# Kernel tuning notes

Hardware: AMD Instinct MI355X
Metric: run time of the kernel (lower is better)

## Reference

```python
import jax, jax.numpy as jnp
import numpy as np

HIDDEN = 512
WINDOW = 32   # window_size: keys span [i-W, i+W]
HEADS = 8
B = 192       # must equal S for the original torch code to run
S = 192


def _split_heads(x, H):
    b, s, e = x.shape
    return x.reshape(b, s, H, e // H)


def _local_window_attn(q, k, v, W):
    """Sliding-window attention: query i attends keys [i-W, i+W] (clipped).
    q,k,v: (B, S, H, D). Chunked (3-neighbor) formulation: K/V duplicated 3x,
    never (2W+1)x. Requires S % W == 0."""
    B_, S_, H_, D_ = q.shape
    C = W
    nc = S_ // C
    qc = q.reshape(B_, nc, C, H_, D_)
    kc = k.reshape(B_, nc, C, H_, D_)
    vc = v.reshape(B_, nc, C, H_, D_)
    pad = ((0, 0), (1, 1), (0, 0), (0, 0), (0, 0))
    kp = jnp.pad(kc, pad)
    vp = jnp.pad(vc, pad)
    # each query chunk sees chunks [n-1, n, n+1] -> (B, nc, 3C, H, D)
    k3 = jnp.concatenate([kp[:, :-2], kp[:, 1:-1], kp[:, 2:]], axis=2)
    v3 = jnp.concatenate([vp[:, :-2], vp[:, 1:-1], vp[:, 2:]], axis=2)
    scale = 1.0 / np.sqrt(D_)
    scores = jnp.einsum('bnqhd,bnkhd->bnhqk', qc, k3) * scale  # (B,nc,H,C,3C)
    # relative key position = (kk - C) - q, independent of chunk index
    rel = jnp.arange(3 * C)[None, :] - C - jnp.arange(C)[:, None]   # (C, 3C)
    band = (rel >= -W) & (rel <= W)
    k_abs = (jnp.arange(nc)[:, None] - 1) * C + jnp.arange(3 * C)[None, :]  # (nc, 3C)
    inb = (k_abs >= 0) & (k_abs < S_)
    valid = band[None, :, :] & inb[:, None, :]                      # (nc, C, 3C)
    scores = jnp.where(valid[:, None, :, :], scores, -jnp.inf)
    attn = jax.nn.softmax(scores, axis=-1)
    out = jnp.einsum('bnhqk,bnkhd->bnqhd', attn, v3)
    return out.reshape(B_, S_, H_ * D_)


def _forward(hidden_states, h_in_w, h_in_b, h_out_w, h_out_b,
             v_in_w, v_in_b, v_out_w, v_out_b,
             mlp_w1, mlp_b1, mlp_w2, mlp_b2):
    x = hidden_states
    W, H = WINDOW, HEADS
    # vertical attention: window slides over the sequence axis (dim 1)
    qv, kv, vv = jnp.split(x @ v_in_w.T + v_in_b, 3, axis=-1)
    v_ctx = _local_window_attn(_split_heads(qv, H), _split_heads(kv, H),
                               _split_heads(vv, H), W)
    v_out = v_ctx @ v_out_w.T + v_out_b
    # horizontal attention: the original slices hidden_states[start:end]
    # (dim 0), so keys for MHA-batch n are x[i-W:i+W+1, n]. Equivalent to
    # sliding-window attention on the (0,1)-transposed K/V (valid since B==S).
    qh, kh, vh = jnp.split(x @ h_in_w.T + h_in_b, 3, axis=-1)
    h_ctx = _local_window_attn(_split_heads(qh, H),
                               _split_heads(kh.swapaxes(0, 1), H),
                               _split_heads(vh.swapaxes(0, 1), H), W)
    h_out = h_ctx @ h_out_w.T + h_out_b
    combined = jnp.concatenate([h_out, v_out], axis=-1)   # (B, S, 2E)
    hid = jax.nn.relu(combined @ mlp_w1.T + mlp_b1)
    return hid @ mlp_w2.T + mlp_b2                         # (B, S, E)


def setup_inputs() -> dict:
    key = jax.random.key(0)
    ks = jax.random.split(key, 8)
    E = HIDDEN
    def w(k, shape):
        return jax.random.normal(k, shape, dtype=jnp.float32) * 0.02
    return {
        'hidden_states': jax.random.normal(ks[0], (B, S, E), dtype=jnp.float32),
        'h_in_w': w(ks[1], (3 * E, E)), 'h_in_b': jnp.zeros((3 * E,), jnp.float32),
        'h_out_w': w(ks[2], (E, E)), 'h_out_b': jnp.zeros((E,), jnp.float32),
        'v_in_w': w(ks[3], (3 * E, E)), 'v_in_b': jnp.zeros((3 * E,), jnp.float32),
        'v_out_w': w(ks[4], (E, E)), 'v_out_b': jnp.zeros((E,), jnp.float32),
        'mlp_w1': w(ks[5], (E, 2 * E)), 'mlp_b1': jnp.zeros((E,), jnp.float32),
        'mlp_w2': w(ks[6], (E, E)), 'mlp_b2': jnp.zeros((E,), jnp.float32),
    }


def reference(hidden_states, h_in_w, h_in_b, h_out_w, h_out_b,
              v_in_w, v_in_b, v_out_w, v_out_b,
              mlp_w1, mlp_b1, mlp_w2, mlp_b2):
    return _forward(hidden_states, h_in_w, h_in_b, h_out_w, h_out_b,
                    v_in_w, v_in_b, v_out_w, v_out_b,
                    mlp_w1, mlp_b1, mlp_w2, mlp_b2)
```

## Files before the change

### kernel.cpp

```cpp
#include <hip/hip_runtime.h>

typedef __bf16 bf16x8 __attribute__((ext_vector_type(8)));
typedef __bf16 bf16x4 __attribute__((ext_vector_type(4)));
typedef float f32x4 __attribute__((ext_vector_type(4)));

__device__ __forceinline__ float bf2f(unsigned short u) {
  union { unsigned int i; float f; } v; v.i = ((unsigned int)u) << 16; return v.f;
}
__device__ __forceinline__ unsigned short f2bf(float f) {
  union { float f; unsigned int i; } v; v.f = f;
  unsigned int u = v.i;
  u += 0x7fffu + ((u >> 16) & 1u);
  return (unsigned short)(u >> 16);
}

#define SB()  __builtin_amdgcn_sched_barrier(0)
#define BAR() __builtin_amdgcn_s_barrier()

__global__ void cvt_all(const float* __restrict__ x,
                        const float* __restrict__ wv, const float* __restrict__ wh,
                        const float* __restrict__ w1, const float* __restrict__ w2,
                        const float* __restrict__ who, const float* __restrict__ wvo,
                        unsigned short* __restrict__ xb, unsigned short* __restrict__ xt,
                        unsigned short* __restrict__ wvb, unsigned short* __restrict__ whb,
                        unsigned short* __restrict__ w1b, unsigned short* __restrict__ w2b,
                        unsigned short* __restrict__ whoT, unsigned short* __restrict__ wvoT)
{
  const int bid = blockIdx.x;
  const int t = threadIdx.x;
  if (bid < 18432) {
    const int ro = bid * 2 + (t >> 7);
    const int idx = t & 127;
    const int s = ro / 192, b = ro - s * 192;
    const int ri = b * 192 + s;
    float4 v = *(const float4*)&x[(size_t)ri * 512 + idx * 4];
    ushort4 o;
    o.x = f2bf(v.x); o.y = f2bf(v.y); o.z = f2bf(v.z); o.w = f2bf(v.w);
    *(ushort4*)&xb[(size_t)ri * 512 + idx * 4] = o;
    *(ushort4*)&xt[(size_t)ro * 512 + idx * 4] = o;
  } else if (bid < 20736) {
    int q = (bid - 18432) * 256 + t;
    const float* src; unsigned short* dst;
    if (q < 196608)      { src = wv;  dst = wvb; }
    else if (q < 393216) { src = wh;  dst = whb; q -= 196608; }
    else if (q < 524288) { src = w1;  dst = w1b; q -= 393216; }
    else                 { src = w2;  dst = w2b; q -= 524288; }
    float4 v = ((const float4*)src)[q];
    ushort4 o;
    o.x = f2bf(v.x); o.y = f2bf(v.y); o.z = f2bf(v.z); o.w = f2bf(v.w);
    ((ushort4*)dst)[q] = o;
  } else {
    const int tb = bid - 20736;
    const float* src = (tb < 256) ? who : wvo;
    unsigned short* dst = (tb < 256) ? whoT : wvoT;
    const int j = (tb & 255) * 2 + (t >> 7);
    const int i0 = (t & 127) * 4;
    ushort4 o;
    o.x = f2bf(src[(size_t)(i0 + 0) * 512 + j]);
    o.y = f2bf(src[(size_t)(i0 + 1) * 512 + j]);
    o.z = f2bf(src[(size_t)(i0 + 2) * 512 + j]);
    o.w = f2bf(src[(size_t)(i0 + 3) * 512 + j]);
    *(ushort4*)&dst[(size_t)j * 512 + i0] = o;
  }
}

__device__ __forceinline__ void async16(const void* g, void* s) {
  __builtin_amdgcn_global_load_lds(
      (const __attribute__((address_space(1))) unsigned int*)g,
      (__attribute__((address_space(3))) unsigned int*)s, 16, 0, 0);
}

__device__ __forceinline__ void fuse_bias_core(int bid,
    const float* b1, const float* hob, const float* vob,
    const float* w1, float* bf)
{
  const int gid = bid * 256 + (int)threadIdx.x;
  const int o = gid >> 4, g = gid & 15;
  if (o < 512) {
    const float* row = w1 + (size_t)o * 1024;
    float s = 0.f;
    #pragma unroll 8
    for (int m = g * 32; m < g * 32 + 32; ++m) s += row[m] * hob[m];
    #pragma unroll 8
    for (int m = g * 32; m < g * 32 + 32; ++m) s += row[512 + m] * vob[m];
    s += __shfl_xor(s, 1);
    s += __shfl_xor(s, 2);
    s += __shfl_xor(s, 4);
    s += __shfl_xor(s, 8);
    if (g == 0) bf[o] = s + b1[o];
  }
}

template<int OUTF32, int RELU, int MODE, int ADDB>
__device__ __forceinline__ void gemm_core(int bid0, int nwg,
    unsigned short* As, unsigned short* Bs,
    const unsigned short* A, const unsigned short* Bt, void* Cv, const float* bias,
    int M, int N, int K, int lda, int ldb, int ldC, int colOff)
{
  const int per = nwg >> 3;
  const int lb = (bid0 & 7) * per + (bid0 >> 3);
  int tm, tn, batch = 0;
  if (MODE == 1) {
    batch = lb >> 3;
    const int sub = lb & 7;
    tm = sub & 3;
    tn = sub >> 2;
  } else {
    const int nb = N >> 7;
    const int grp = lb / (4 * nb);
    const int r = lb - grp * 4 * nb;
    tm = grp * 4 + (r & 3);
    tn = r >> 2;
  }
  const int t = threadIdx.x;
  const int w = t >> 6, l = t & 63;
  const int wr = w >> 1, wc = w & 1;
  const int lr = l & 15, kg = l >> 4;

  const unsigned short* Abase = A + (size_t)tm * 128 * lda;
  const unsigned short* Bbase = (MODE == 1)
      ? Bt + ((size_t)batch * 192 + tn * 64) * ldb
      : Bt + (size_t)tn * 128 * ldb;

  const int r0 = t >> 2;
  const int s0 = (((t & 3) ^ ((t >> 3) & 3))) * 8;
  const size_t ga0 = (size_t)r0 * lda + s0;
  const size_t ga1 = (size_t)(64 + r0) * lda + s0;
  const size_t gb0 = (size_t)r0 * ldb + s0;
  const size_t gb1 = (size_t)(64 + r0) * ldb + s0;
  const int ldsoff = w * 512;

  const f32x4 zero4 = {0.f, 0.f, 0.f, 0.f};
  f32x4 acc[4][4];
  #pragma unroll
  for (int m = 0; m < 4; ++m)
    #pragma unroll
    for (int n = 0; n < 4; ++n) acc[m][n] = zero4;

  auto stage = [&](int kt, int slot) {
    async16(Abase + ga0 + kt, &As[slot * 4096 + ldsoff]);
    async16(Abase + ga1 + kt, &As[slot * 4096 + 2048 + ldsoff]);
    async16(Bbase + gb0 + kt, &Bs[slot * 4096 + ldsoff]);
    async16(Bbase + gb1 + kt, &Bs[slot * 4096 + 2048 + ldsoff]);
  };

  const int nk = K >> 5;
  stage(0, 0);
  stage(32, 1);

  const int rsw = (kg ^ ((lr >> 1) & 3)) * 8;

  int cur = 0;
  for (int it = 0; it < nk; ++it) {
    if (it + 1 < nk) asm volatile("s_waitcnt vmcnt(4)" ::: "memory");
    else             asm volatile("s_waitcnt vmcnt(0)" ::: "memory");
    SB(); BAR(); SB();

    int st = cur + 2; if (st >= 3) st -= 3;
    if (it + 2 < nk) stage((it + 2) << 5, st);

    bf16x8 af[4], bfv[4];
    #pragma unroll
    for (int m = 0; m < 4; ++m)
      af[m] = *(const bf16x8*)&As[cur * 4096 + (wr * 64 + m * 16 + lr) * 32 + rsw];
    #pragma unroll
    for (int n = 0; n < 4; ++n)
      bfv[n] = *(const bf16x8*)&Bs[cur * 4096 + (wc * 64 + n * 16 + lr) * 32 + rsw];
    #pragma unroll
    for (int m = 0; m < 4; ++m)
      #pragma unroll
      for (int n = 0; n < 4; ++n)
        acc[m][n] = __builtin_amdgcn_mfma_f32_16x16x32_bf16(af[m], bfv[n],
                                                            acc[m][n], 0, 0, 0);
    cur = cur + 1; if (cur >= 3) cur = 0;
  }

  const int row0 = tm * 128 + wr * 64;
  const int colL0 = (MODE == 1) ? (tn * 64 + wc * 64) : (tn * 128 + wc * 64);

  if (MODE == 1) {
    unsigned short* Cw = (unsigned short*)Cv + (size_t)batch * 98304;
    #pragma unroll
    for (int m = 0; m < 4; ++m) {
      const int rowb = row0 + m * 16 + kg * 4;
      float4 bv4 = {0.f, 0.f, 0.f, 0.f};
      if (ADDB) bv4 = *(const float4*)&bias[rowb];
      #pragma unroll
      for (int rr = 0; rr < 4; ++rr) {
        const float bv = ((const float*)&bv4)[rr];
        const size_t rbase = (size_t)(rowb + rr) * 192;
        #pragma unroll
        for (int n = 0; n < 4; ++n) {
          const int j = colL0 + n * 16 + lr;
          Cw[rbase + j] = f2bf(acc[m][n][rr] + bv);
        }
      }
    }
    return;
  }

  #pragma unroll
  for (int n = 0; n < 4; ++n) {
    const int ccol = colL0 + n * 16 + lr;
    const float bv = ADDB ? bias[ccol] : 0.f;
    #pragma unroll
    for (int m = 0; m < 4; ++m) {
      #pragma unroll
      for (int r = 0; r < 4; ++r) {
        const int crow = row0 + m * 16 + kg * 4 + r;
        float v = acc[m][n][r] + bv;
        if (RELU) v = fmaxf(v, 0.f);
        if (OUTF32)
          ((float*)Cv)[(size_t)crow * ldC + colOff + ccol] = v;
        else
          ((unsigned short*)Cv)[(size_t)crow * ldC + colOff + ccol] = f2bf(v);
      }
    }
  }
}

template<int OUTF32, int RELU, int MODE, int ADDB>
__global__ __launch_bounds__(256, 3)
void gemm_bt(const unsigned short* __restrict__ A,
             const unsigned short* __restrict__ Bt,
             void* __restrict__ Cv, const float* __restrict__ bias,
             int M, int N, int K, int lda, int ldb, int ldC, int colOff)
{
  __shared__ unsigned short smem[3 * 4096 * 2];
  gemm_core<OUTF32, RELU, MODE, ADDB>((int)blockIdx.x, (int)gridDim.x,
                                      smem, smem + 12288,
                                      A, Bt, Cv, bias, M, N, K, lda, ldb, ldC, colOff);
}

__global__ __launch_bounds__(256, 3)
void proj_h(const unsigned short* __restrict__ xb, const unsigned short* __restrict__ xt,
            const unsigned short* __restrict__ whb,
            const unsigned short* __restrict__ w1b,
            const unsigned short* __restrict__ whoT, const unsigned short* __restrict__ wvoT,
            unsigned short* __restrict__ vto, unsigned short* __restrict__ qko,
            unsigned short* __restrict__ G, float* __restrict__ bfz,
            const float* __restrict__ h_in_b,
            const float* __restrict__ b1, const float* __restrict__ hob,
            const float* __restrict__ vob, const float* __restrict__ w1f)
{
  __shared__ unsigned short smem[3 * 4096 * 2];
  const int bid = (int)blockIdx.x;
  if (bid < 1536)
    gemm_core<0,0,1,1>(bid, 1536, smem, smem + 12288, whb + 1024 * 512, xt, vto,
                       h_in_b + 1024, 512, 192, 512, 512, 512, 192, 0);
  else if (bid < 3840)
    gemm_core<0,0,0,1>(bid - 1536, 2304, smem, smem + 12288, xb, whb, qko,
                       h_in_b, 36864, 1024, 512, 512, 512, 1024, 0);
  else if (bid < 3856)
    gemm_core<0,0,0,0>(bid - 3840, 16, smem, smem + 12288, w1b, whoT, G,
                       bfz, 512, 512, 512, 1024, 512, 1024, 0);
  else if (bid < 3872)
    gemm_core<0,0,0,0>(bid - 3856, 16, smem, smem + 12288, w1b + 512, wvoT, G,
                       bfz, 512, 512, 512, 1024, 512, 1024, 512);
  else
    fuse_bias_core(bid - 3872, b1, hob, vob, w1f, bfz);
}

__global__ __launch_bounds__(256, 3)
void proj_v(const unsigned short* __restrict__ xb,
            const unsigned short* __restrict__ wvb,
            unsigned short* __restrict__ vto, unsigned short* __restrict__ qko,
            const float* __restrict__ v_in_b)
{
  __shared__ unsigned short smem[3 * 4096 * 2];
  const int bid = (int)blockIdx.x;
  if (bid < 1536)
    gemm_core<0,0,1,1>(bid, 1536, smem, smem + 12288, wvb + 1024 * 512, xb, vto,
                       v_in_b + 1024, 512, 192, 512, 512, 512, 192, 0);
  else
    gemm_core<0,0,0,1>(bid - 1536, 2304, smem, smem + 12288, xb, wvb, qko,
                       v_in_b, 36864, 1024, 512, 512, 512, 1024, 0);
}

__global__ __launch_bounds__(256)
void attn_mfma(const unsigned short* __restrict__ qk,
               const unsigned short* __restrict__ vt,
               unsigned short* __restrict__ ctx, int hbranch, int ldc, int colOff)
{
  __shared__ unsigned short P_lds[4][32 * 104];
  __shared__ float rinv[4][32];

  const int t = threadIdx.x;
  const int w = t >> 6, l = t & 63;
  const int lr = l & 15, kg = l >> 4;
  const int bid = blockIdx.x;
  const int hg = bid & 1;
  const int n = (bid >> 1) % 6;
  const int b = bid / 12;
  const int h = hg * 4 + w;
  const int kabase = (n - 1) * 32;

  bf16x8 qf[2][2];
  #pragma unroll
  for (int ct = 0; ct < 2; ++ct)
    #pragma unroll
    for (int ks = 0; ks < 2; ++ks)
      qf[ct][ks] = *(const bf16x8*)&qk[(size_t)(b * 192 + n * 32 + ct * 16 + lr) * 1024
                                       + h * 64 + ks * 32 + kg * 8];

  const f32x4 z4 = {0.f, 0.f, 0.f, 0.f};
  f32x4 sacc[6][2];
  #pragma unroll
  for (int mt = 0; mt < 6; ++mt) { sacc[mt][0] = z4; sacc[mt][1] = z4; }

  #pragma unroll
  for (int mt = 0; mt < 6; ++mt) {
    int ka = kabase + mt * 16 + lr;
    ka = ka < 0 ? 0 : (ka > 191 ? 191 : ka);
    const size_t row = hbranch ? (size_t)ka * 192 + b : (size_t)b * 192 + ka;
    #pragma unroll
    for (int ks = 0; ks < 2; ++ks) {
      bf16x8 kf = *(const bf16x8*)&qk[row * 1024 + 512 + h * 64 + ks * 32 + kg * 8];
      #pragma unroll
      for (int ct = 0; ct < 2; ++ct)
        sacc[mt][ct] = __builtin_amdgcn_mfma_f32_16x16x32_bf16(kf, qf[ct][ks],
                                                               sacc[mt][ct], 0, 0, 0);
    }
  }

  bf16x8 vf[4][3];
  #pragma unroll
  for (int dt = 0; dt < 4; ++dt)
    #pragma unroll
    for (int t2 = 0; t2 < 3; ++t2) {
      int ka0 = kabase + t2 * 32 + kg * 8;
      if (ka0 < 0 || ka0 > 184) ka0 = 0;
      vf[dt][t2] = *(const bf16x8*)&vt[((size_t)(b * 8 + h) * 64 + dt * 16 + lr) * 192 + ka0];
    }

  unsigned short* Pw = &P_lds[w][0];
  #pragma unroll
  for (int ct = 0; ct < 2; ++ct) {
    const int q = ct * 16 + lr;
    float mx = -1e30f;
    #pragma unroll
    for (int mt = 0; mt < 6; ++mt)
      #pragma unroll
      for (int rr = 0; rr < 4; ++rr) {
        const int kk = mt * 16 + kg * 4 + rr;
        const int ka = kabase + kk;
        const bool valid = (kk >= q) && (kk <= q + 64) && (ka >= 0) && (ka < 192);
        const float s = valid ? sacc[mt][ct][rr] : -1e30f;
        sacc[mt][ct][rr] = s;
        mx = fmaxf(mx, s);
      }
    mx = fmaxf(mx, __shfl_xor(mx, 16));
    mx = fmaxf(mx, __shfl_xor(mx, 32));
    float sum = 0.f;
    #pragma unroll
    for (int mt = 0; mt < 6; ++mt) {
      bf16x4 pk;
      #pragma unroll
      for (int rr = 0; rr < 4; ++rr) {
        const float e = exp2f((sacc[mt][ct][rr] - mx) * 0.1803368801111137f);
        sum += e;
        pk[rr] = (__bf16)e;
      }
      *(bf16x4*)&Pw[q * 104 + mt * 16 + kg * 4] = pk;
    }
    sum += __shfl_xor(sum, 16);
    sum += __shfl_xor(sum, 32);
    if (kg == 0) rinv[w][q] = 1.0f / sum;
  }

  f32x4 oacc[2][4];
  #pragma unroll
  for (int mq = 0; mq < 2; ++mq)
    #pragma unroll
    for (int dt = 0; dt < 4; ++dt) oacc[mq][dt] = z4;

  #pragma unroll
  for (int t2 = 0; t2 < 3; ++t2)
    #pragma unroll
    for (int mq = 0; mq < 2; ++mq) {
      bf16x8 pa = *(const bf16x8*)&Pw[(mq * 16 + lr) * 104 + t2 * 32 + kg * 8];
      #pragma unroll
      for (int dt = 0; dt < 4; ++dt)
        oacc[mq][dt] = __builtin_amdgcn_mfma_f32_16x16x32_bf16(pa, vf[dt][t2],
                                                               oacc[mq][dt], 0, 0, 0);
    }

  #pragma unroll
  for (int mq = 0; mq < 2; ++mq)
    #pragma unroll
    for (int rr = 0; rr < 4; ++rr) {
      const int q = mq * 16 + kg * 4 + rr;
      const float rv = rinv[w][q];
      const size_t row = (size_t)(b * 192 + n * 32 + q) * ldc + colOff + h * 64;
      #pragma unroll
      for (int dt = 0; dt < 4; ++dt)
        ctx[row + dt * 16 + lr] = f2bf(oacc[mq][dt][rr] * rv);
    }
}

extern "C" void kernel_launch(void* const* d_in, const int* in_sizes, int n_in,
                              void* d_out, int out_size, void* d_ws, size_t ws_size,
                              hipStream_t stream) {
  const float* x       = (const float*)d_in[0];
  const float* h_in_w  = (const float*)d_in[1];
  const float* h_in_b  = (const float*)d_in[2];
  const float* h_out_w = (const float*)d_in[3];
  const float* h_out_b = (const float*)d_in[4];
  const float* v_in_w  = (const float*)d_in[5];
  const float* v_in_b  = (const float*)d_in[6];
  const float* v_out_w = (const float*)d_in[7];
  const float* v_out_b = (const float*)d_in[8];
  const float* w1      = (const float*)d_in[9];
  const float* b1      = (const float*)d_in[10];
  const float* w2      = (const float*)d_in[11];
  const float* b2      = (const float*)d_in[12];

  const size_t XB   = 0;
  const size_t WVB  = 37748736;
  const size_t WHB  = 39321600;
  const size_t WHOT = 40894464;
  const size_t WVOT = 41418752;
  const size_t W1B  = 41943040;
  const size_t W2B  = 42991616;
  const size_t CTX2 = 43515904;
  const size_t QKO  = 119013376;
  const size_t VTO  = 194510848;
  const size_t NEED = 232259584;
  if (ws_size < NEED) return;

  char* ws = (char*)d_ws;
  unsigned short* xb   = (unsigned short*)(ws + XB);
  unsigned short* wvb  = (unsigned short*)(ws + WVB);
  unsigned short* whb  = (unsigned short*)(ws + WHB);
  unsigned short* whoT = (unsigned short*)(ws + WHOT);
  unsigned short* wvoT = (unsigned short*)(ws + WVOT);
  unsigned short* w1b  = (unsigned short*)(ws + W1B);
  unsigned short* w2b  = (unsigned short*)(ws + W2B);
  unsigned short* ctx2 = (unsigned short*)(ws + CTX2);
  unsigned short* xt   = (unsigned short*)(ws + CTX2);
  unsigned short* qko  = (unsigned short*)(ws + QKO);
  unsigned short* vto  = (unsigned short*)(ws + VTO);
  unsigned short* hid  = (unsigned short*)(ws + QKO);
  unsigned short* G    = (unsigned short*)d_out;
  float*          bfz  = (float*)((char*)d_out + 1048576);

  cvt_all<<<21248, 256, 0, stream>>>(x, v_in_w, h_in_w, w1, w2, h_out_w, v_out_w,
                                     xb, xt, wvb, whb, w1b, w2b, whoT, wvoT);
  proj_h<<<3904, 256, 0, stream>>>(xb, xt, whb, w1b, whoT, wvoT, vto, qko,
                                   G, bfz, h_in_b, b1, h_out_b, v_out_b, w1);
  attn_mfma<<<192 * 6 * 2, 256, 0, stream>>>(qko, vto, ctx2, 1, 1024, 0);
  proj_v<<<3840, 256, 0, stream>>>(xb, wvb, vto, qko, v_in_b);
  attn_mfma<<<192 * 6 * 2, 256, 0, stream>>>(qko, vto, ctx2, 0, 1024, 512);
  gemm_bt<0,1,0,1><<<288 * 4, 256, 0, stream>>>(ctx2, G, hid, bfz,
                                                36864, 512, 1024, 1024, 1024, 512, 0);
  gemm_bt<1,0,0,1><<<288 * 4, 256, 0, stream>>>(hid, w2b, d_out, b2,
                                                36864, 512, 512, 512, 512, 512, 0);
}
```

Before: 356.1 us.

## Compute V-transpose projection as one large GEMM with row bias instead of batched tiles

The V projection (W_v · x^T) was computed as a batched GEMM with 192 batches of 512x192 outputs using 128x64 tiles. It is now a single 512x36864 GEMM with full 128x128 tiles and a row-indexed bias, stored in a [h*64+d][b*192+s] layout. The attention kernel's V loads are updated to the new layout. This removes the half-width tiles and batch-indexing overhead, so fewer workgroups are launched with better MFMA utilisation. In exchange, the V reads in attention now stride across a larger matrix, and the row bias is loaded per element.

```diff
diff --git a/kernel.cpp b/kernel.cpp
--- a/kernel.cpp
+++ b/kernel.cpp
@@ -91,7 +91,7 @@
   }
 }
 
-template<int OUTF32, int RELU, int MODE, int ADDB>
+template<int OUTF32, int RELU, int BIASROW, int ADDB>
 __device__ __forceinline__ void gemm_core(int bid0, int nwg,
     unsigned short* As, unsigned short* Bs,
     const unsigned short* A, const unsigned short* Bt, void* Cv, const float* bias,
@@ -99,28 +99,19 @@
 {
   const int per = nwg >> 3;
   const int lb = (bid0 & 7) * per + (bid0 >> 3);
-  int tm, tn, batch = 0;
-  if (MODE == 1) {
-    batch = lb >> 3;
-    const int sub = lb & 7;
-    tm = sub & 3;
-    tn = sub >> 2;
-  } else {
-    const int nb = N >> 7;
-    const int grp = lb / (4 * nb);
-    const int r = lb - grp * 4 * nb;
-    tm = grp * 4 + (r & 3);
-    tn = r >> 2;
-  }
+  const int nb = N >> 7;
+  const int grp = lb / (4 * nb);
+  const int r = lb - grp * 4 * nb;
+  const int tm = grp * 4 + (r & 3);
+  const int tn = r >> 2;
+
   const int t = threadIdx.x;
   const int w = t >> 6, l = t & 63;
   const int wr = w >> 1, wc = w & 1;
   const int lr = l & 15, kg = l >> 4;
 
   const unsigned short* Abase = A + (size_t)tm * 128 * lda;
-  const unsigned short* Bbase = (MODE == 1)
-      ? Bt + ((size_t)batch * 192 + tn * 64) * ldb
-      : Bt + (size_t)tn * 128 * ldb;
+  const unsigned short* Bbase = Bt + (size_t)tn * 128 * ldb;
 
   const int r0 = t >> 2;
   const int s0 = (((t & 3) ^ ((t >> 3) & 3))) * 8;
@@ -176,39 +167,18 @@
   }
 
   const int row0 = tm * 128 + wr * 64;
-  const int colL0 = (MODE == 1) ? (tn * 64 + wc * 64) : (tn * 128 + wc * 64);
-
-  if (MODE == 1) {
-    unsigned short* Cw = (unsigned short*)Cv + (size_t)batch * 98304;
-    #pragma unroll
-    for (int m = 0; m < 4; ++m) {
-      const int rowb = row0 + m * 16 + kg * 4;
-      float4 bv4 = {0.f, 0.f, 0.f, 0.f};
-      if (ADDB) bv4 = *(const float4*)&bias[rowb];
-      #pragma unroll
-      for (int rr = 0; rr < 4; ++rr) {
-        const float bv = ((const float*)&bv4)[rr];
-        const size_t rbase = (size_t)(rowb + rr) * 192;
-        #pragma unroll
-        for (int n = 0; n < 4; ++n) {
-          const int j = colL0 + n * 16 + lr;
-          Cw[rbase + j] = f2bf(acc[m][n][rr] + bv);
-        }
-      }
-    }
-    return;
-  }
+  const int colL0 = tn * 128 + wc * 64;
 
   #pragma unroll
   for (int n = 0; n < 4; ++n) {
     const int ccol = colL0 + n * 16 + lr;
-    const float bv = ADDB ? bias[ccol] : 0.f;
+    const float bvc = (ADDB && !BIASROW) ? bias[ccol] : 0.f;
     #pragma unroll
     for (int m = 0; m < 4; ++m) {
       #pragma unroll
-      for (int r = 0; r < 4; ++r) {
-        const int crow = row0 + m * 16 + kg * 4 + r;
-        float v = acc[m][n][r] + bv;
+      for (int r2 = 0; r2 < 4; ++r2) {
+        const int crow = row0 + m * 16 + kg * 4 + r2;
+        float v = acc[m][n][r2] + ((ADDB && BIASROW) ? bias[crow] : bvc);
         if (RELU) v = fmaxf(v, 0.f);
         if (OUTF32)
           ((float*)Cv)[(size_t)crow * ldC + colOff + ccol] = v;
@@ -219,7 +189,7 @@
   }
 }
 
-template<int OUTF32, int RELU, int MODE, int ADDB>
+template<int OUTF32, int RELU, int BIASROW, int ADDB>
 __global__ __launch_bounds__(256, 3)
 void gemm_bt(const unsigned short* __restrict__ A,
              const unsigned short* __restrict__ Bt,
@@ -227,9 +197,9 @@
              int M, int N, int K, int lda, int ldb, int ldC, int colOff)
 {
   __shared__ unsigned short smem[3 * 4096 * 2];
-  gemm_core<OUTF32, RELU, MODE, ADDB>((int)blockIdx.x, (int)gridDim.x,
-                                      smem, smem + 12288,
-                                      A, Bt, Cv, bias, M, N, K, lda, ldb, ldC, colOff);
+  gemm_core<OUTF32, RELU, BIASROW, ADDB>((int)blockIdx.x, (int)gridDim.x,
+                                         smem, smem + 12288,
+                                         A, Bt, Cv, bias, M, N, K, lda, ldb, ldC, colOff);
 }
 
 __global__ __launch_bounds__(256, 3)
@@ -245,20 +215,20 @@
 {
   __shared__ unsigned short smem[3 * 4096 * 2];
   const int bid = (int)blockIdx.x;
-  if (bid < 1536)
-    gemm_core<0,0,1,1>(bid, 1536, smem, smem + 12288, whb + 1024 * 512, xt, vto,
-                       h_in_b + 1024, 512, 192, 512, 512, 512, 192, 0);
-  else if (bid < 3840)
-    gemm_core<0,0,0,1>(bid - 1536, 2304, smem, smem + 12288, xb, whb, qko,
+  if (bid < 1152)
+    gemm_core<0,0,1,1>(bid, 1152, smem, smem + 12288, whb + 1024 * 512, xt, vto,
+                       h_in_b + 1024, 512, 36864, 512, 512, 512, 36864, 0);
+  else if (bid < 3456)
+    gemm_core<0,0,0,1>(bid - 1152, 2304, smem, smem + 12288, xb, whb, qko,
                        h_in_b, 36864, 1024, 512, 512, 512, 1024, 0);
-  else if (bid < 3856)
-    gemm_core<0,0,0,0>(bid - 3840, 16, smem, smem + 12288, w1b, whoT, G,
+  else if (bid < 3472)
+    gemm_core<0,0,0,0>(bid - 3456, 16, smem, smem + 12288, w1b, whoT, G,
                        bfz, 512, 512, 512, 1024, 512, 1024, 0);
-  else if (bid < 3872)
-    gemm_core<0,0,0,0>(bid - 3856, 16, smem, smem + 12288, w1b + 512, wvoT, G,
+  else if (bid < 3488)
+    gemm_core<0,0,0,0>(bid - 3472, 16, smem, smem + 12288, w1b + 512, wvoT, G,
                        bfz, 512, 512, 512, 1024, 512, 1024, 512);
   else
-    fuse_bias_core(bid - 3872, b1, hob, vob, w1f, bfz);
+    fuse_bias_core(bid - 3488, b1, hob, vob, w1f, bfz);
 }
 
 __global__ __launch_bounds__(256, 3)
@@ -269,11 +239,11 @@
 {
   __shared__ unsigned short smem[3 * 4096 * 2];
   const int bid = (int)blockIdx.x;
-  if (bid < 1536)
-    gemm_core<0,0,1,1>(bid, 1536, smem, smem + 12288, wvb + 1024 * 512, xb, vto,
-                       v_in_b + 1024, 512, 192, 512, 512, 512, 192, 0);
+  if (bid < 1152)
+    gemm_core<0,0,1,1>(bid, 1152, smem, smem + 12288, wvb + 1024 * 512, xb, vto,
+                       v_in_b + 1024, 512, 36864, 512, 512, 512, 36864, 0);
   else
-    gemm_core<0,0,0,1>(bid - 1536, 2304, smem, smem + 12288, xb, wvb, qko,
+    gemm_core<0,0,0,1>(bid - 1152, 2304, smem, smem + 12288, xb, wvb, qko,
                        v_in_b, 36864, 1024, 512, 512, 512, 1024, 0);
 }
 
@@ -330,7 +300,8 @@
     for (int t2 = 0; t2 < 3; ++t2) {
       int ka0 = kabase + t2 * 32 + kg * 8;
       if (ka0 < 0 || ka0 > 184) ka0 = 0;
-      vf[dt][t2] = *(const bf16x8*)&vt[((size_t)(b * 8 + h) * 64 + dt * 16 + lr) * 192 + ka0];
+      vf[dt][t2] = *(const bf16x8*)&vt[(size_t)(h * 64 + dt * 16 + lr) * 36864
+                                       + b * 192 + ka0];
     }
 
   unsigned short* Pw = &P_lds[w][0];
@@ -446,10 +417,10 @@
 
   cvt_all<<<21248, 256, 0, stream>>>(x, v_in_w, h_in_w, w1, w2, h_out_w, v_out_w,
                                      xb, xt, wvb, whb, w1b, w2b, whoT, wvoT);
-  proj_h<<<3904, 256, 0, stream>>>(xb, xt, whb, w1b, whoT, wvoT, vto, qko,
+  proj_h<<<3520, 256, 0, stream>>>(xb, xt, whb, w1b, whoT, wvoT, vto, qko,
                                    G, bfz, h_in_b, b1, h_out_b, v_out_b, w1);
   attn_mfma<<<192 * 6 * 2, 256, 0, stream>>>(qko, vto, ctx2, 1, 1024, 0);
-  proj_v<<<3840, 256, 0, stream>>>(xb, wvb, vto, qko, v_in_b);
+  proj_v<<<3456, 256, 0, stream>>>(xb, wvb, vto, qko, v_in_b);
   attn_mfma<<<192 * 6 * 2, 256, 0, stream>>>(qko, vto, ctx2, 0, 1024, 512);
   gemm_bt<0,1,0,1><<<288 * 4, 256, 0, stream>>>(ctx2, G, hid, bfz,
                                                 36864, 512, 1024, 1024, 1024, 512, 0);
```

Result: faster. 343.9 us (median of 3 runs) (-3.4%).
